# Performance work log

Hardware: AMD Instinct MI355X
Metric: run time of the kernel (lower is better)

The kernel has to match this reference:

```python
import jax, jax.numpy as jnp
from jax import lax
import numpy as np

BLUR = 1e-4      # sinkhorn_blur
P_NORM = 2       # sinkhorn_p
SCALING = 0.9
NUM_SG = 8
LOCAL_W = 1.0
GLOBAL_W = 0.5
BATCH = 4096
DIM = 256


def _cost(X, Y):
    # geomloss cost for p=2: ||x-y||^2 / 2, computed via GEMM (no [P,m,m,d] broadcast)
    x2 = jnp.sum(X * X, axis=-1)                      # [P,m]
    y2 = jnp.sum(Y * Y, axis=-1)                      # [P,m]
    xy = jnp.einsum('pid,pjd->pij', X, Y)             # [P,m,m]
    sq = jnp.clip(x2[:, :, None] + y2[:, None, :] - 2.0 * xy, 0.0)
    return 0.5 * sq


def _softmin(eps, C, h):
    # softmin_eps(C, h)_i = -eps * logsumexp_j (h_j - C_ij / eps)
    return -eps * jax.nn.logsumexp(h[:, None, :] - C / eps, axis=-1)


def _eps_schedule():
    # epsilon-scaling: from (diameter bound)^p down to blur^p by factor scaling^p
    eps0 = 4.0 * DIM                 # static upper bound on sq. diameter of N(0,1) features
    target = BLUR ** P_NORM
    ratio = SCALING ** P_NORM
    n = int(np.ceil(np.log(target / eps0) / np.log(ratio)))
    return np.maximum(eps0 * ratio ** np.arange(n + 1), target).astype(np.float32)


def _sinkhorn_pairs(X, Y):
    # Debiased Sinkhorn divergence for a batch of pairs; X,Y: [P,m,d] -> [P]
    P, m, d = X.shape
    loga = -jnp.log(float(m))  # uniform weights
    Cxy = _cost(X, Y)
    Cyx = jnp.swapaxes(Cxy, 1, 2)
    Cxx = _cost(X, X)
    Cyy = _cost(Y, Y)
    # geomloss runs the scaling iterations detached, then one last extrapolation with grad
    Cs = tuple(lax.stop_gradient(C) for C in (Cxy, Cyx, Cxx, Cyy))
    eps_list = jnp.asarray(_eps_schedule())

    def body(carry, eps):
        f, g, px, py = carry
        ft = _softmin(eps, Cs[0], loga + g / eps)
        gt = _softmin(eps, Cs[1], loga + f / eps)
        pxt = _softmin(eps, Cs[2], loga + px / eps)
        pyt = _softmin(eps, Cs[3], loga + py / eps)
        return (0.5 * (f + ft), 0.5 * (g + gt), 0.5 * (px + pxt), 0.5 * (py + pyt)), None

    init = tuple(jnp.zeros((P, m), X.dtype) for _ in range(4))
    (f, g, px, py), _ = lax.scan(body, init, eps_list)

    eps_f = eps_list[-1]
    f_fin = _softmin(eps_f, Cxy, loga + lax.stop_gradient(g) / eps_f)
    g_fin = _softmin(eps_f, Cyx, loga + lax.stop_gradient(f) / eps_f)
    px_fin = _softmin(eps_f, Cxx, loga + lax.stop_gradient(px) / eps_f)
    py_fin = _softmin(eps_f, Cyy, loga + lax.stop_gradient(py) / eps_f)
    # S_eps(x,y) = <a, f - p_x> + <b, g - p_y>, uniform weights -> means
    return jnp.mean(f_fin - px_fin, axis=-1) + jnp.mean(g_fin - py_fin, axis=-1)


def _forward(features, labels, subgroups):
    B, d = features.shape
    m_local = B // (2 * NUM_SG)   # samples per (class, subgroup) cell
    m_global = B // NUM_SG        # samples per subgroup
    pi, pj = np.triu_indices(NUM_SG, k=1)  # 28 subgroup pairs

    # local: per-class subgroup cells (balanced inputs -> static sizes)
    cells = []
    for lbl in range(2):
        for sg in range(NUM_SG):
            idx = jnp.nonzero((labels == lbl) & (subgroups == sg), size=m_local)[0]
            cells.append(features[idx])
    cells = jnp.stack(cells).reshape(2, NUM_SG, m_local, d)
    X = cells[:, pi].reshape(-1, m_local, d)   # [56,m,d]
    Y = cells[:, pj].reshape(-1, m_local, d)
    # (sum_real/28 + sum_fake/28)/2 == mean over all 56 pairs
    local_loss = jnp.mean(_sinkhorn_pairs(X, Y))

    gcells = jnp.stack([features[jnp.nonzero(subgroups == sg, size=m_global)[0]]
                        for sg in range(NUM_SG)])  # [8,m_g,d]
    global_loss = jnp.mean(_sinkhorn_pairs(gcells[pi], gcells[pj]))

    return LOCAL_W * local_loss + GLOBAL_W * global_loss


def setup_inputs():
    key = jax.random.key(0)
    features = jax.random.normal(key, (BATCH, DIM), dtype=jnp.float32)
    ar = jnp.arange(BATCH, dtype=jnp.int32)
    labels = ar % 2                      # balanced real/fake
    subgroups = (ar // 2) % NUM_SG       # balanced subgroups per class
    return {"features": features, "labels": labels, "subgroups": subgroups}


def reference(features, labels, subgroups):
    return _forward(features, labels, subgroups)
```

## Files before the change

kernel.cpp:

```cpp
#include <hip/hip_runtime.h>
#include <math.h>

#define LOG2E 1.4426950408889634f
#define LN2   0.6931471805599453f

typedef short    short8  __attribute__((ext_vector_type(8)));
typedef float    floatx4 __attribute__((ext_vector_type(4)));
typedef _Float16 half8   __attribute__((ext_vector_type(8)));

__constant__ int c_pi[28] = {0,0,0,0,0,0,0,1,1,1,1,1,1,2,2,2,2,2,3,3,3,3,4,4,4,5,5,6};
__constant__ int c_pj[28] = {1,2,3,4,5,6,7,2,3,4,5,6,7,3,4,5,6,7,4,5,6,7,5,6,7,6,7,7};

__device__ unsigned short g_cellsL[16*256*256];
__device__ unsigned short g_cellsG[8*512*256];
__device__ float g_x2L[16*256];
__device__ float g_x2G[8*512];
__device__ int   g_idxL[16*256];
__device__ int   g_idxG[8*512];
__device__ _Float16 g_CL[128*256*256];
__device__ _Float16 g_CG[64*512*512];
__device__ float g_fL[2][56*256];
__device__ float g_gL[2][56*256];
__device__ float g_pxL[2][16*256];
__device__ float g_fG[2][28*512];
__device__ float g_gG[2][28*512];
__device__ float g_pxG[2][8*512];

__device__ __forceinline__ unsigned short f2bf(float f) {
    unsigned u = __float_as_uint(f);
    u += 0x7fffu + ((u >> 16) & 1u);
    return (unsigned short)(u >> 16);
}

__global__ void k_index(const int* __restrict__ labels, const int* __restrict__ subg) {
    int b = blockIdx.x, lane = threadIdx.x;
    int want_l, want_s, cap; int* out;
    if (b < 16) { want_l = b >> 3; want_s = b & 7; cap = 256; out = g_idxL + b*256; }
    else        { want_l = -1;     want_s = b - 16; cap = 512; out = g_idxG + (b-16)*512; }
    int cnt = 0;
    for (int base = 0; base < 4096; base += 64) {
        int i = base + lane;
        bool m = (subg[i] == want_s) && (want_l < 0 || labels[i] == want_l);
        unsigned long long mask = __ballot(m);
        int pos = cnt + __popcll(mask & ((1ull << lane) - 1ull));
        if (m && pos < cap) out[pos] = i;
        cnt += __popcll(mask);
    }
}

__global__ void k_gather(const float* __restrict__ feat) {
    int wv = blockIdx.x*4 + (threadIdx.x >> 6);
    int lane = threadIdx.x & 63;
    const float* src; unsigned short* dst; float* x2out;
    if (wv < 4096) {
        int c = wv >> 8, row = wv & 255;
        src = feat + (size_t)g_idxL[c*256+row]*256;
        dst = g_cellsL + (size_t)(c*256+row)*256;
        x2out = g_x2L + c*256 + row;
    } else {
        int v = wv - 4096; int c = v >> 9, row = v & 511;
        src = feat + (size_t)g_idxG[c*512+row]*256;
        dst = g_cellsG + (size_t)(c*512+row)*256;
        x2out = g_x2G + c*512 + row;
    }
    floatx4 v4 = *(const floatx4*)(src + lane*4);
    float s = v4[0]*v4[0] + v4[1]*v4[1] + v4[2]*v4[2] + v4[3]*v4[3];
    unsigned lo = (unsigned)f2bf(v4[0]) | ((unsigned)f2bf(v4[1]) << 16);
    unsigned hi = (unsigned)f2bf(v4[2]) | ((unsigned)f2bf(v4[3]) << 16);
    unsigned* d32 = (unsigned*)dst;
    d32[lane*2] = lo; d32[lane*2+1] = hi;
    for (int o = 32; o; o >>= 1) s += __shfl_xor(s, o);
    if (lane == 0) *x2out = s;
}

__global__ void k_gemm() {
    int job = blockIdx.x*4 + (threadIdx.x >> 6);
    int lane = threadIdx.x & 63;
    const unsigned short *A, *B; _Float16* Cout; const float *x2a, *x2b;
    int m, ti, tj;
    if (job < 32768) {
        int mm = job >> 8, t = job & 255; ti = t >> 4; tj = t & 15; m = 256;
        int ca, cb;
        if (mm < 56)       { int lbl = mm/28,  q = mm%28;  ca = lbl*8 + c_pi[q]; cb = lbl*8 + c_pj[q]; }
        else if (mm < 112) { int p = mm-56; int lbl = p/28, q = p%28;
                             ca = lbl*8 + c_pj[q]; cb = lbl*8 + c_pi[q]; }
        else               { int c = mm-112; ca = cb = c; }
        A = g_cellsL + (size_t)ca*65536; B = g_cellsL + (size_t)cb*65536;
        x2a = g_x2L + ca*256; x2b = g_x2L + cb*256;
        Cout = g_CL + (size_t)mm*65536;
    } else {
        int jj = job - 32768; int mm = jj >> 10, t = jj & 1023; ti = t >> 5; tj = t & 31; m = 512;
        int ca, cb;
        if (mm < 28)      { ca = c_pi[mm];    cb = c_pj[mm]; }
        else if (mm < 56) { ca = c_pj[mm-28]; cb = c_pi[mm-28]; }
        else              { ca = cb = mm-56; }
        A = g_cellsG + (size_t)ca*131072; B = g_cellsG + (size_t)cb*131072;
        x2a = g_x2G + ca*512; x2b = g_x2G + cb*512;
        Cout = g_CG + (size_t)mm*262144;
    }
    int r = lane & 15, quad = lane >> 4;
    const unsigned short* Ap = A + (size_t)(ti*16 + r)*256 + quad*8;
    const unsigned short* Bp = B + (size_t)(tj*16 + r)*256 + quad*8;
    floatx4 acc = {0.f, 0.f, 0.f, 0.f};
    #pragma unroll
    for (int k = 0; k < 256; k += 32) {
        short8 av = *(const short8*)(Ap + k);
        short8 bv = *(const short8*)(Bp + k);
        acc = __builtin_amdgcn_mfma_f32_16x16x32_bf16(av, bv, acc, 0, 0, 0);
    }
    int jc = tj*16 + r;
    float y2 = x2b[jc];
    #pragma unroll
    for (int rr = 0; rr < 4; rr++) {
        int ir = ti*16 + quad*4 + rr;
        float v = x2a[ir] + y2 - 2.f*acc[rr];
        Cout[(size_t)ir*m + jc] = (_Float16)(0.5f*fmaxf(v, 0.f));
    }
}

__global__ void k_init() {
    int t = blockIdx.x*256 + threadIdx.x;
    if      (t < 14336) g_fL[0][t] = 0.f;
    else if (t < 28672) g_gL[0][t-14336] = 0.f;
    else if (t < 32768) g_pxL[0][t-28672] = 0.f;
    else if (t < 47104) g_fG[0][t-32768] = 0.f;
    else if (t < 61440) g_gG[0][t-47104] = 0.f;
    else                g_pxG[0][t-61440] = 0.f;
}

template<int M>
__device__ __forceinline__ void sm_pass(const _Float16* __restrict__ C,
    const float* __restrict__ hsrc, const float* __restrict__ fold,
    float* __restrict__ fout, int r0, float eps, float inv_eps, float loga,
    int hard, int fin)
{
    const int W = (M == 256) ? 16 : 32;
    int tid = threadIdx.x, lane = tid & 63, w = tid >> 6;
    int co = (M == 256) ? (lane & 31) : lane;
    float h[8];
    floatx4 h0 = *(const floatx4*)(hsrc + co*8);
    floatx4 h1 = *(const floatx4*)(hsrc + co*8 + 4);
    #pragma unroll
    for (int k = 0; k < 4; k++) { h[k] = loga + h0[k]*inv_eps; h[4+k] = loga + h1[k]*inv_eps; }
    int rbase = (M == 256) ? (r0 + w*16) : (r0 + w*8);
    int rowst = (M == 256) ? 2 : 1;
    int radd  = (M == 256) ? (lane >> 5) : 0;
    bool wr   = (M == 256) ? ((lane & 31) == 0) : (lane == 0);

    const _Float16* cp = C + (size_t)(rbase + radd)*M + co*8;
    half8 cv = *(const half8*)cp;
    #pragma unroll
    for (int s = 0; s < 8; s++) {
        half8 cvn;
        if (s < 7) cvn = *(const half8*)(cp + (size_t)rowst*M);
        float tv[8]; float mx = -3.4e38f;
        #pragma unroll
        for (int k = 0; k < 8; k++) {
            float t = h[k] - (float)cv[k]*inv_eps;
            tv[k] = t; mx = fmaxf(mx, t);
        }
        #pragma unroll
        for (int o = W; o; o >>= 1) mx = fmaxf(mx, __shfl_xor(mx, o));
        float ft;
        if (!hard) {
            float sum = 0.f;
            #pragma unroll
            for (int k = 0; k < 8; k++) sum += exp2f((tv[k] - mx)*LOG2E);
            #pragma unroll
            for (int o = W; o; o >>= 1) sum += __shfl_xor(sum, o);
            ft = -eps*(mx + LN2*__log2f(sum));
        } else {
            ft = -eps*mx;
        }
        if (wr) {
            int row = rbase + rowst*s + radd;
            fout[row] = fin ? ft : 0.5f*(fold[row] + ft);
        }
        cv = cvn; cp += (size_t)rowst*M;
    }
}

__global__ void k_iter(float eps, float inv_eps, int par, int hard, int fin) {
    const float LGA = -5.545177444479562f;
    const float LGG = -6.238324625039508f;
    int b = blockIdx.x;
    int po = par, pn = par ^ 1;
    if (b < 512) {
        int m = b >> 2, r0 = (b & 3)*64;
        const _Float16* C = g_CL + (size_t)m*65536;
        const float *h, *fo; float* fn;
        if (m < 56)       { h = g_gL[po]+m*256;  fo = g_fL[po]+m*256;  fn = g_fL[pn]+m*256; }
        else if (m < 112) { int p = m-56;  h = g_fL[po]+p*256;  fo = g_gL[po]+p*256;  fn = g_gL[pn]+p*256; }
        else              { int c = m-112; h = g_pxL[po]+c*256; fo = h;               fn = g_pxL[pn]+c*256; }
        sm_pass<256>(C, h, fo, fn, r0, eps, inv_eps, LGA, hard, fin);
    } else {
        int v = b - 512; int m = v >> 4, r0 = (v & 15)*32;
        const _Float16* C = g_CG + (size_t)m*262144;
        const float *h, *fo; float* fn;
        if (m < 28)      { h = g_gG[po]+m*512;  fo = g_fG[po]+m*512;  fn = g_fG[pn]+m*512; }
        else if (m < 56) { int p = m-28;  h = g_fG[po]+p*512;  fo = g_gG[po]+p*512;  fn = g_gG[pn]+p*512; }
        else             { int c = m-56;  h = g_pxG[po]+c*512; fo = h;               fn = g_pxG[pn]+c*512; }
        sm_pass<512>(C, h, fo, fn, r0, eps, inv_eps, LGG, hard, fin);
    }
}

__global__ void k_combine(float* __restrict__ out) {
    __shared__ float red[4][4];
    int tid = threadIdx.x;
    float sfg_l = 0.f, spx_l = 0.f, sfg_g = 0.f, spx_g = 0.f;
    for (int i = tid; i < 14336; i += 256) sfg_l += g_fL[1][i] + g_gL[1][i];
    for (int i = tid; i < 4096;  i += 256) spx_l += g_pxL[1][i];
    for (int i = tid; i < 14336; i += 256) sfg_g += g_fG[1][i] + g_gG[1][i];
    for (int i = tid; i < 4096;  i += 256) spx_g += g_pxG[1][i];
    for (int o = 32; o; o >>= 1) {
        sfg_l += __shfl_xor(sfg_l, o); spx_l += __shfl_xor(spx_l, o);
        sfg_g += __shfl_xor(sfg_g, o); spx_g += __shfl_xor(spx_g, o);
    }
    int w = tid >> 6;
    if ((tid & 63) == 0) { red[0][w] = sfg_l; red[1][w] = spx_l; red[2][w] = sfg_g; red[3][w] = spx_g; }
    __syncthreads();
    if (tid == 0) {
        float SL = red[0][0]+red[0][1]+red[0][2]+red[0][3];
        float PL = red[1][0]+red[1][1]+red[1][2]+red[1][3];
        float SG = red[2][0]+red[2][1]+red[2][2]+red[2][3];
        float PG = red[3][0]+red[3][1]+red[3][2]+red[3][3];
        float local_l  = SL/14336.f - PL/2048.f;
        float global_l = SG/14336.f - PG/2048.f;
        out[0] = 1.0f*local_l + 0.5f*global_l;
    }
}

extern "C" void kernel_launch(void* const* d_in, const int* in_sizes, int n_in,
                              void* d_out, int out_size, void* d_ws, size_t ws_size,
                              hipStream_t stream) {
    (void)in_sizes; (void)n_in; (void)out_size; (void)d_ws; (void)ws_size;
    const float* feat  = (const float*)d_in[0];
    const int* labels  = (const int*)d_in[1];
    const int* subg    = (const int*)d_in[2];

    k_index <<<24,    64, 0, stream>>>(labels, subg);
    k_gather<<<2048, 256, 0, stream>>>(feat);
    k_gemm  <<<24576,256, 0, stream>>>();
    k_init  <<<256,  256, 0, stream>>>();

    double eps0 = 4.0*256.0, ratio = 0.9*0.9, target = 1e-4*1e-4;
    int n = (int)ceil(log(target/eps0)/log(ratio));
    float ef = 1e-8f;
    for (int k = 0; k <= n; k++) {
        double e = eps0 * pow(ratio, (double)k);
        if (e < target) e = target;
        ef = (float)e;
        int hard = (ef < 1e-5f) ? 1 : 0;
        k_iter<<<1536, 256, 0, stream>>>(ef, (float)(1.0/(double)ef), k & 1, hard, 0);
    }
    k_iter<<<1536, 256, 0, stream>>>(ef, (float)(1.0/(double)ef), 0, 1, 1);
    k_combine<<<1, 256, 0, stream>>>((float*)d_out);
}
```

Baseline: 2.019 ms.

## Fuse Sinkhorn iterations into one persistent kernel with per-pair atomic barriers

Replaces the roughly 123 per-epsilon kernel launches with a single persistent kernel. Each block owns a row slice of one cost matrix, keeps part of it resident in LDS, and synchronises with the other blocks of the same matrix through global atomic counters between iterations. The previous potentials stay in registers instead of being reread from memory. The GEMM is also reorganised so each block computes a 64x64 tile and stages B in shared memory for reuse. This removes launch overhead and repeated cost-matrix streaming, but it relies on all 768 blocks being co-resident, otherwise the spin barriers can deadlock.

```diff
diff --git a/kernel.cpp b/kernel.cpp
--- a/kernel.cpp
+++ b/kernel.cpp
@@ -3,6 +3,8 @@
 
 #define LOG2E 1.4426950408889634f
 #define LN2   0.6931471805599453f
+#define LGA  -5.545177444479562f
+#define LGG  -6.238324625039508f
 
 typedef short    short8  __attribute__((ext_vector_type(8)));
 typedef float    floatx4 __attribute__((ext_vector_type(4)));
@@ -25,6 +27,7 @@
 __device__ float g_fG[2][28*512];
 __device__ float g_gG[2][28*512];
 __device__ float g_pxG[2][8*512];
+__device__ unsigned g_ctr[108];
 
 __device__ __forceinline__ unsigned short f2bf(float f) {
     unsigned u = __float_as_uint(f);
@@ -73,13 +76,13 @@
     if (lane == 0) *x2out = s;
 }
 
-__global__ void k_gemm() {
-    int job = blockIdx.x*4 + (threadIdx.x >> 6);
-    int lane = threadIdx.x & 63;
+__global__ __launch_bounds__(256) void k_gemm() {
+    __shared__ _Float16 sB[16384];
+    int b = blockIdx.x, tid = threadIdx.x, lane = tid & 63, w = tid >> 6;
     const unsigned short *A, *B; _Float16* Cout; const float *x2a, *x2b;
-    int m, ti, tj;
-    if (job < 32768) {
-        int mm = job >> 8, t = job & 255; ti = t >> 4; tj = t & 15; m = 256;
+    int m, tI, tJ;
+    if (b < 2048) {
+        int mm = b >> 4, t = b & 15; tI = t >> 2; tJ = t & 3; m = 256;
         int ca, cb;
         if (mm < 56)       { int lbl = mm/28,  q = mm%28;  ca = lbl*8 + c_pi[q]; cb = lbl*8 + c_pj[q]; }
         else if (mm < 112) { int p = mm-56; int lbl = p/28, q = p%28;
@@ -89,7 +92,7 @@
         x2a = g_x2L + ca*256; x2b = g_x2L + cb*256;
         Cout = g_CL + (size_t)mm*65536;
     } else {
-        int jj = job - 32768; int mm = jj >> 10, t = jj & 1023; ti = t >> 5; tj = t & 31; m = 512;
+        int v = b - 2048; int mm = v >> 6, t = v & 63; tI = t >> 3; tJ = t & 7; m = 512;
         int ca, cb;
         if (mm < 28)      { ca = c_pi[mm];    cb = c_pj[mm]; }
         else if (mm < 56) { ca = c_pj[mm-28]; cb = c_pi[mm-28]; }
@@ -98,28 +101,39 @@
         x2a = g_x2G + ca*512; x2b = g_x2G + cb*512;
         Cout = g_CG + (size_t)mm*262144;
     }
+    const unsigned short* Bp0 = B + (size_t)(tJ*64)*256;
+    for (int i = tid; i < 2048; i += 256) {
+        int j = i >> 5, c8 = i & 31, kk = c8 >> 2, q = c8 & 3;
+        *(short8*)(sB + (size_t)((kk*64 + j)*4 + q)*8) = *(const short8*)(Bp0 + j*256 + c8*8);
+    }
     int r = lane & 15, quad = lane >> 4;
-    const unsigned short* Ap = A + (size_t)(ti*16 + r)*256 + quad*8;
-    const unsigned short* Bp = B + (size_t)(tj*16 + r)*256 + quad*8;
-    floatx4 acc = {0.f, 0.f, 0.f, 0.f};
+    const unsigned short* Ap = A + (size_t)(tI*64 + w*16 + r)*256 + quad*8;
+    short8 a[8];
     #pragma unroll
-    for (int k = 0; k < 256; k += 32) {
-        short8 av = *(const short8*)(Ap + k);
-        short8 bv = *(const short8*)(Bp + k);
-        acc = __builtin_amdgcn_mfma_f32_16x16x32_bf16(av, bv, acc, 0, 0, 0);
-    }
-    int jc = tj*16 + r;
-    float y2 = x2b[jc];
+    for (int kk = 0; kk < 8; kk++) a[kk] = *(const short8*)(Ap + kk*32);
+    __syncthreads();
     #pragma unroll
-    for (int rr = 0; rr < 4; rr++) {
-        int ir = ti*16 + quad*4 + rr;
-        float v = x2a[ir] + y2 - 2.f*acc[rr];
-        Cout[(size_t)ir*m + jc] = (_Float16)(0.5f*fmaxf(v, 0.f));
+    for (int tj = 0; tj < 4; tj++) {
+        floatx4 acc = {0.f, 0.f, 0.f, 0.f};
+        #pragma unroll
+        for (int kk = 0; kk < 8; kk++) {
+            short8 bv = *(const short8*)(sB + (size_t)((kk*64 + tj*16 + r)*4 + quad)*8);
+            acc = __builtin_amdgcn_mfma_f32_16x16x32_bf16(a[kk], bv, acc, 0, 0, 0);
+        }
+        int jc = tJ*64 + tj*16 + r;
+        float y2 = x2b[jc];
+        #pragma unroll
+        for (int rr = 0; rr < 4; rr++) {
+            int ir = tI*64 + w*16 + quad*4 + rr;
+            float v = x2a[ir] + y2 - 2.f*acc[rr];
+            Cout[(size_t)ir*m + jc] = (_Float16)(0.5f*fmaxf(v, 0.f));
+        }
     }
 }
 
 __global__ void k_init() {
     int t = blockIdx.x*256 + threadIdx.x;
+    if (t < 108) g_ctr[t] = 0;
     if      (t < 14336) g_fL[0][t] = 0.f;
     else if (t < 28672) g_gL[0][t-14336] = 0.f;
     else if (t < 32768) g_pxL[0][t-28672] = 0.f;
@@ -129,78 +143,130 @@
 }
 
 template<int M>
-__device__ __forceinline__ void sm_pass(const _Float16* __restrict__ C,
-    const float* __restrict__ hsrc, const float* __restrict__ fold,
-    float* __restrict__ fout, int r0, float eps, float inv_eps, float loga,
-    int hard, int fin)
+__device__ void run_unit(const _Float16* __restrict__ Cmat, _Float16* sC,
+                         int rb, float* fv0, float* fv1,
+                         const float* hv0, const float* hv1,
+                         unsigned* ctr, int gsize, float loga)
 {
-    const int W = (M == 256) ? 16 : 32;
+    const int LR = (M == 256) ? 80 : 40;
+    const int W0 = (M == 256) ? 16 : 32;
     int tid = threadIdx.x, lane = tid & 63, w = tid >> 6;
     int co = (M == 256) ? (lane & 31) : lane;
-    float h[8];
-    floatx4 h0 = *(const floatx4*)(hsrc + co*8);
-    floatx4 h1 = *(const floatx4*)(hsrc + co*8 + 4);
+    int rsel = (M == 256) ? (lane >> 5) : 0;
+
+    {
+        const short8* src8 = (const short8*)(Cmat + (size_t)rb*M);
+        short8* dst8 = (short8*)sC;
+        for (int i = tid; i < 2560; i += 256) dst8[i] = src8[i];
+    }
+    __syncthreads();
+
+    float fprev[16];
     #pragma unroll
-    for (int k = 0; k < 4; k++) { h[k] = loga + h0[k]*inv_eps; h[4+k] = loga + h1[k]*inv_eps; }
-    int rbase = (M == 256) ? (r0 + w*16) : (r0 + w*8);
-    int rowst = (M == 256) ? 2 : 1;
-    int radd  = (M == 256) ? (lane >> 5) : 0;
-    bool wr   = (M == 256) ? ((lane & 31) == 0) : (lane == 0);
-
-    const _Float16* cp = C + (size_t)(rbase + radd)*M + co*8;
-    half8 cv = *(const half8*)cp;
-    #pragma unroll
-    for (int s = 0; s < 8; s++) {
-        half8 cvn;
-        if (s < 7) cvn = *(const half8*)(cp + (size_t)rowst*M);
-        float tv[8]; float mx = -3.4e38f;
+    for (int s = 0; s < 16; s++) fprev[s] = 0.f;
+
+    double e = 1024.0;
+    unsigned tgt = 0;
+    for (int k = 0; k < 123; k++) {
+        bool fin = (k == 122);
+        double ed = (e < 1e-8) ? 1e-8 : e;
+        e *= 0.81;
+        float eps = (float)ed;
+        float inv_eps = (float)(1.0/ed);
+        int po = fin ? 0 : (k & 1);
+        bool hard = (eps < 1e-5f);
+        const float* hs = po ? hv1 : hv0;
+        float* fn = po ? fv0 : fv1;
+
+        float h[8];
         #pragma unroll
-        for (int k = 0; k < 8; k++) {
-            float t = h[k] - (float)cv[k]*inv_eps;
-            tv[k] = t; mx = fmaxf(mx, t);
+        for (int q = 0; q < 8; q++) {
+            float hq = __hip_atomic_load((float*)&hs[co*8 + q],
+                                         __ATOMIC_RELAXED, __HIP_MEMORY_SCOPE_AGENT);
+            h[q] = loga + hq*inv_eps;
         }
         #pragma unroll
-        for (int o = W; o; o >>= 1) mx = fmaxf(mx, __shfl_xor(mx, o));
-        float ft;
-        if (!hard) {
-            float sum = 0.f;
+        for (int s = 0; s < 16; s++) {
+            int row = (M == 256) ? (w*32 + s*2 + rsel) : (w*16 + s);
+            half8 cv;
+            if (row < LR) cv = *(const half8*)(sC + (size_t)row*M + co*8);
+            else          cv = *(const half8*)(Cmat + (size_t)(rb + row)*M + co*8);
+            float tv[8]; float mx = -3.4e38f;
             #pragma unroll
-            for (int k = 0; k < 8; k++) sum += exp2f((tv[k] - mx)*LOG2E);
+            for (int q = 0; q < 8; q++) {
+                float t = fmaf(-(float)cv[q], inv_eps, h[q]);
+                tv[q] = t; mx = fmaxf(mx, t);
+            }
             #pragma unroll
-            for (int o = W; o; o >>= 1) sum += __shfl_xor(sum, o);
-            ft = -eps*(mx + LN2*__log2f(sum));
+            for (int o = W0; o; o >>= 1) mx = fmaxf(mx, __shfl_xor(mx, o));
+            float ft;
+            if (!hard) {
+                float sum = 0.f;
+                #pragma unroll
+                for (int q = 0; q < 8; q++) sum += exp2f((tv[q] - mx)*LOG2E);
+                #pragma unroll
+                for (int o = W0; o; o >>= 1) sum += __shfl_xor(sum, o);
+                ft = -eps*(mx + LN2*__log2f(sum));
+            } else {
+                ft = -eps*mx;
+            }
+            float fnew = fin ? ft : 0.5f*(fprev[s] + ft);
+            fprev[s] = fnew;
+            if (co == 0)
+                __hip_atomic_store(&fn[rb + row], fnew,
+                                   __ATOMIC_RELAXED, __HIP_MEMORY_SCOPE_AGENT);
+        }
+        if (!fin) {
+            tgt += (unsigned)gsize;
+            __syncthreads();
+            if (tid == 0) {
+                __hip_atomic_fetch_add(ctr, 1u, __ATOMIC_RELEASE, __HIP_MEMORY_SCOPE_AGENT);
+                while (__hip_atomic_load(ctr, __ATOMIC_ACQUIRE, __HIP_MEMORY_SCOPE_AGENT) < tgt)
+                    __builtin_amdgcn_s_sleep(1);
+            }
+            __syncthreads();
+        }
+    }
+}
+
+__global__ __launch_bounds__(256, 3) void k_sink() {
+    __shared__ _Float16 sC[20480];
+    int b = blockIdx.x;
+    if (b < 512) {
+        const _Float16* Cm; float *f0, *f1; const float *h0, *h1;
+        unsigned* ct; int gs, rb;
+        if (b < 448) {
+            int side = (b >= 224); int v = side ? b - 224 : b;
+            int p = v >> 3, j = v & 7; rb = j*64;
+            Cm = g_CG + (size_t)(side ? 28 + p : p)*262144;
+            if (!side) { h0 = g_gG[0]+p*512; h1 = g_gG[1]+p*512; f0 = g_fG[0]+p*512; f1 = g_fG[1]+p*512; }
+            else       { h0 = g_fG[0]+p*512; h1 = g_fG[1]+p*512; f0 = g_gG[0]+p*512; f1 = g_gG[1]+p*512; }
+            ct = g_ctr + p; gs = 16;
         } else {
-            ft = -eps*mx;
-        }
-        if (wr) {
-            int row = rbase + rowst*s + radd;
-            fout[row] = fin ? ft : 0.5f*(fold[row] + ft);
-        }
-        cv = cvn; cp += (size_t)rowst*M;
-    }
-}
-
-__global__ void k_iter(float eps, float inv_eps, int par, int hard, int fin) {
-    const float LGA = -5.545177444479562f;
-    const float LGG = -6.238324625039508f;
-    int b = blockIdx.x;
-    int po = par, pn = par ^ 1;
-    if (b < 512) {
-        int m = b >> 2, r0 = (b & 3)*64;
-        const _Float16* C = g_CL + (size_t)m*65536;
-        const float *h, *fo; float* fn;
-        if (m < 56)       { h = g_gL[po]+m*256;  fo = g_fL[po]+m*256;  fn = g_fL[pn]+m*256; }
-        else if (m < 112) { int p = m-56;  h = g_fL[po]+p*256;  fo = g_gL[po]+p*256;  fn = g_gL[pn]+p*256; }
-        else              { int c = m-112; h = g_pxL[po]+c*256; fo = h;               fn = g_pxL[pn]+c*256; }
-        sm_pass<256>(C, h, fo, fn, r0, eps, inv_eps, LGA, hard, fin);
+            int v = b - 448; int c = v >> 3, j = v & 7; rb = j*64;
+            Cm = g_CG + (size_t)(56 + c)*262144;
+            h0 = g_pxG[0]+c*512; h1 = g_pxG[1]+c*512; f0 = g_pxG[0]+c*512; f1 = g_pxG[1]+c*512;
+            ct = g_ctr + 28 + c; gs = 8;
+        }
+        run_unit<512>(Cm, sC, rb, f0, f1, h0, h1, ct, gs, LGG);
     } else {
-        int v = b - 512; int m = v >> 4, r0 = (v & 15)*32;
-        const _Float16* C = g_CG + (size_t)m*262144;
-        const float *h, *fo; float* fn;
-        if (m < 28)      { h = g_gG[po]+m*512;  fo = g_fG[po]+m*512;  fn = g_fG[pn]+m*512; }
-        else if (m < 56) { int p = m-28;  h = g_fG[po]+p*512;  fo = g_gG[po]+p*512;  fn = g_gG[pn]+p*512; }
-        else             { int c = m-56;  h = g_pxG[po]+c*512; fo = h;               fn = g_pxG[pn]+c*512; }
-        sm_pass<512>(C, h, fo, fn, r0, eps, inv_eps, LGG, hard, fin);
+        const _Float16* Cm; float *f0, *f1; const float *h0, *h1;
+        unsigned* ct; int gs, rb;
+        int v = b - 512;
+        if (v < 224) {
+            int side = (v >= 112); int u = side ? v - 112 : v;
+            int p = u >> 1, j = u & 1; rb = j*128;
+            Cm = g_CL + (size_t)(side ? 56 + p : p)*65536;
+            if (!side) { h0 = g_gL[0]+p*256; h1 = g_gL[1]+p*256; f0 = g_fL[0]+p*256; f1 = g_fL[1]+p*256; }
+            else       { h0 = g_fL[0]+p*256; h1 = g_fL[1]+p*256; f0 = g_gL[0]+p*256; f1 = g_gL[1]+p*256; }
+            ct = g_ctr + 36 + p; gs = 4;
+        } else {
+            int u = v - 224; int c = u >> 1, j = u & 1; rb = j*128;
+            Cm = g_CL + (size_t)(112 + c)*65536;
+            h0 = g_pxL[0]+c*256; h1 = g_pxL[1]+c*256; f0 = g_pxL[0]+c*256; f1 = g_pxL[1]+c*256;
+            ct = g_ctr + 92 + c; gs = 2;
+        }
+        run_unit<256>(Cm, sC, rb, f0, f1, h0, h1, ct, gs, LGA);
     }
 }
 
@@ -238,21 +304,10 @@
     const int* labels  = (const int*)d_in[1];
     const int* subg    = (const int*)d_in[2];
 
-    k_index <<<24,    64, 0, stream>>>(labels, subg);
-    k_gather<<<2048, 256, 0, stream>>>(feat);
-    k_gemm  <<<24576,256, 0, stream>>>();
-    k_init  <<<256,  256, 0, stream>>>();
-
-    double eps0 = 4.0*256.0, ratio = 0.9*0.9, target = 1e-4*1e-4;
-    int n = (int)ceil(log(target/eps0)/log(ratio));
-    float ef = 1e-8f;
-    for (int k = 0; k <= n; k++) {
-        double e = eps0 * pow(ratio, (double)k);
-        if (e < target) e = target;
-        ef = (float)e;
-        int hard = (ef < 1e-5f) ? 1 : 0;
-        k_iter<<<1536, 256, 0, stream>>>(ef, (float)(1.0/(double)ef), k & 1, hard, 0);
-    }
-    k_iter<<<1536, 256, 0, stream>>>(ef, (float)(1.0/(double)ef), 0, 1, 1);
-    k_combine<<<1, 256, 0, stream>>>((float*)d_out);
-}
+    k_index  <<<24,    64, 0, stream>>>(labels, subg);
+    k_gather <<<2048, 256, 0, stream>>>(feat);
+    k_gemm   <<<6144, 256, 0, stream>>>();
+    k_init   <<<256,  256, 0, stream>>>();
+    k_sink   <<<768,  256, 0, stream>>>();
+    k_combine<<<1,    256, 0, stream>>>((float*)d_out);
+}
```

After: 7.778 ms. +285.3%, slower.
